# Performance work log

Hardware: AMD Instinct MI355X
Metric: run time of the kernel (lower is better)

Reference implementation:

```python
import jax, jax.numpy as jnp
import numpy as np


def setup_inputs() -> dict:
    key = jax.random.key(0)
    k1, k2 = jax.random.split(key)
    # x: [B, D, H, W, C] 3D latent grid, C == embedding_dim
    x = jax.random.normal(k1, (4, 32, 32, 16, 256), dtype=jnp.float32)
    # codebook stored as (embedding_dim, num_embeddings) like the TF variable
    embeddings = jax.random.uniform(k2, (256, 4096), dtype=jnp.float32)
    return {"x": x, "embeddings": embeddings}


def reference(x, embeddings):
    # Inference-mode forward of VectorQuantizer.call (training=False).
    D, K = embeddings.shape  # (embedding_dim, num_embeddings)
    flat = x.reshape(-1, D)  # [N, D]
    # squared L2 distances: ||z||^2 + ||e||^2 - 2 z.e  -> [N, K]
    sim = flat @ embeddings
    dist = (jnp.sum(flat * flat, axis=1, keepdims=True)
            + jnp.sum(embeddings * embeddings, axis=0)
            - 2.0 * sim)
    idx = jnp.argmin(dist, axis=1)  # [N]
    # nearest-codebook lookup (gather codebook columns)
    quantized = jnp.take(embeddings.T, idx, axis=0).reshape(x.shape)
    # perplexity from code usage histogram (avoids materializing [N,K] one-hot)
    n = flat.shape[0]
    counts = jnp.zeros((K,), dtype=jnp.float32).at[idx].add(1.0)
    avg_probs = counts / n
    perplexity = jnp.exp(-jnp.sum(avg_probs * jnp.log(avg_probs + 1e-10)))
    return quantized, perplexity
```

## Files before the change

### kernel.cpp

```cpp
#include <hip/hip_runtime.h>
#include <hip/hip_bf16.h>

#define NROWS 65536
#define DIM   256
#define KCB   4096
#define CHUNK 32
#define NCH   (KCB / CHUNK)
#define NBUF  4
#define BUFB  16384
#define NENHB 16384

typedef __attribute__((ext_vector_type(8))) short bf16x8;
typedef __attribute__((ext_vector_type(4))) float f32x4;

#define WAITV(n) asm volatile("s_waitcnt vmcnt(" #n ")" ::: "memory")

__device__ inline short f2bf(float f) {
    __hip_bfloat16 h = __float2bfloat16(f);
    return *reinterpret_cast<short*>(&h);
}

__global__ void prep_transpose(const float* __restrict__ E,
                               float* __restrict__ ET32,
                               ushort* __restrict__ ETbf)
{
    __shared__ float tile[64][65];
    const int kb = blockIdx.x * 64;
    const int db = blockIdx.y * 64;
    const int lo = threadIdx.x & 63;
    const int hi = threadIdx.x >> 6;

#pragma unroll
    for (int i = 0; i < 16; ++i) {
        int d = i * 4 + hi;
        tile[lo][d] = E[(size_t)(db + d) * KCB + kb + lo];
    }
    __syncthreads();
#pragma unroll
    for (int i = 0; i < 16; ++i) {
        int k = i * 4 + hi;
        float v = tile[k][lo];
        size_t off = (size_t)(kb + k) * DIM + db + lo;
        ET32[off] = v;
        ETbf[off] = (ushort)f2bf(v);
    }
}

__global__ void prep_enorm(const float* __restrict__ E, float* __restrict__ nenh)
{
    int k = blockIdx.x * 256 + threadIdx.x;
    float s = 0.0f;
#pragma unroll 8
    for (int d = 0; d < DIM; ++d) {
        float v = E[(size_t)d * KCB + k];
        s = fmaf(v, v, s);
    }
    nenh[k] = -0.5f * s;
}

__shared__ char lds_raw[NENHB + NBUF * BUFB];

template <int BUF>
__device__ __forceinline__ void stage_chunk(
    const char* __restrict__ etb, const int (&soff)[4], int wave, int ct)
{
    const char* base = etb + (size_t)ct * (CHUNK * 512);
#pragma unroll
    for (int j = 0; j < 4; ++j) {
        __builtin_amdgcn_global_load_lds(
            (const __attribute__((address_space(1))) unsigned*)(base + soff[j]),
            (__attribute__((address_space(3))) unsigned*)
                (lds_raw + NENHB + BUF * BUFB + wave * 4096 + j * 1024),
            16, 0, 0);
    }
}

template <int BUF>
__device__ __forceinline__ void process_chunk(
    const bf16x8 (&afrag)[2][8],
    const int (&boffB)[8],
    float (&best)[2][4], int (&bidx)[2][4],
    int l15, int ct)
{
    const float* nlds = (const float*)lds_raw;
#pragma unroll
    for (int tc = 0; tc < 2; ++tc) {
        const int col = ct * CHUNK + tc * 16 + l15;
        const float nh = nlds[ct * CHUNK + tc * 16 + l15];
        f32x4 acc0 = {nh, nh, nh, nh};
        f32x4 acc1 = {nh, nh, nh, nh};
        bf16x8 bfr[8];
#pragma unroll
        for (int kc = 0; kc < 8; ++kc)
            bfr[kc] = *(const bf16x8*)(lds_raw + boffB[kc]
                                       + BUF * BUFB + tc * 8192);
        __builtin_amdgcn_s_setprio(1);
#pragma unroll
        for (int kc = 0; kc < 8; ++kc) {
            acc0 = __builtin_amdgcn_mfma_f32_16x16x32_bf16(
                afrag[0][kc], bfr[kc], acc0, 0, 0, 0);
            acc1 = __builtin_amdgcn_mfma_f32_16x16x32_bf16(
                afrag[1][kc], bfr[kc], acc1, 0, 0, 0);
        }
        __builtin_amdgcn_s_setprio(0);
#pragma unroll
        for (int r = 0; r < 4; ++r) {
            float s0 = acc0[r];
            bool g0 = s0 > best[0][r];
            bidx[0][r] = g0 ? col : bidx[0][r];
            best[0][r] = fmaxf(best[0][r], s0);
            float s1 = acc1[r];
            bool g1 = s1 > best[1][r];
            bidx[1][r] = g1 ? col : bidx[1][r];
            best[1][r] = fmaxf(best[1][r], s1);
        }
    }
}

__global__ __launch_bounds__(256, 2)
void vq_argmin(const float* __restrict__ X,
               const ushort* __restrict__ ETbf,
               const float* __restrict__ nenh,
               int* __restrict__ idxout)
{
    const int tid  = threadIdx.x;
    const int lane = tid & 63;
    const int wave = tid >> 6;
    const int l15  = lane & 15;
    const int g    = lane >> 4;
    const int m    = l15 & 7;
    const long rowbase = (long)blockIdx.x * 128 + wave * 32;

    int soff[4];
#pragma unroll
    for (int j = 0; j < 4; ++j) {
        const int o    = wave * 4096 + j * 1024 + lane * 16;
        const int col0 = o >> 9;
        const int cph  = (o >> 4) & 31;
        soff[j] = (col0 << 9) + ((cph ^ (col0 & 7)) << 4);
    }

#pragma unroll
    for (int j = 0; j < 4; ++j) {
        int o = wave * 4096 + j * 1024 + lane * 16;
        __builtin_amdgcn_global_load_lds(
            (const __attribute__((address_space(1))) unsigned*)((const char*)nenh + o),
            (__attribute__((address_space(3))) unsigned*)
                (lds_raw + wave * 4096 + j * 1024),
            16, 0, 0);
    }
    stage_chunk<0>((const char*)ETbf, soff, wave, 0);
    stage_chunk<1>((const char*)ETbf, soff, wave, 1);
    stage_chunk<2>((const char*)ETbf, soff, wave, 2);

    bf16x8 afrag[2][8];
#pragma unroll
    for (int rt = 0; rt < 2; ++rt) {
        const float* xr = X + (rowbase + rt * 16 + l15) * DIM;
#pragma unroll
        for (int kc = 0; kc < 8; ++kc) {
            int k0 = g * 64 + kc * 8;
            float4 v0 = *(const float4*)(xr + k0);
            float4 v1 = *(const float4*)(xr + k0 + 4);
            bf16x8 f;
            f[0] = f2bf(v0.x); f[1] = f2bf(v0.y);
            f[2] = f2bf(v0.z); f[3] = f2bf(v0.w);
            f[4] = f2bf(v1.x); f[5] = f2bf(v1.y);
            f[6] = f2bf(v1.z); f[7] = f2bf(v1.w);
            afrag[rt][kc] = f;
        }
    }

    int boffB[8];
#pragma unroll
    for (int kc = 0; kc < 8; ++kc)
        boffB[kc] = NENHB + l15 * 512 + ((((g << 3) + kc) ^ m) << 4);

    float best[2][4];
    int   bidx[2][4];
#pragma unroll
    for (int rt = 0; rt < 2; ++rt)
#pragma unroll
        for (int r = 0; r < 4; ++r) { best[rt][r] = -3.4e38f; bidx[rt][r] = 0x7fffffff; }

    const char* etb = (const char*)ETbf;

    for (int gq = 0; gq < 31; ++gq) {
        const int ct = gq * 4;
        WAITV(8); __builtin_amdgcn_s_barrier();
        stage_chunk<3>(etb, soff, wave, ct + 3);
        process_chunk<0>(afrag, boffB, best, bidx, l15, ct);
        WAITV(8); __builtin_amdgcn_s_barrier();
        stage_chunk<0>(etb, soff, wave, ct + 4);
        process_chunk<1>(afrag, boffB, best, bidx, l15, ct + 1);
        WAITV(8); __builtin_amdgcn_s_barrier();
        stage_chunk<1>(etb, soff, wave, ct + 5);
        process_chunk<2>(afrag, boffB, best, bidx, l15, ct + 2);
        WAITV(8); __builtin_amdgcn_s_barrier();
        stage_chunk<2>(etb, soff, wave, ct + 6);
        process_chunk<3>(afrag, boffB, best, bidx, l15, ct + 3);
    }
    WAITV(8); __builtin_amdgcn_s_barrier();
    stage_chunk<3>(etb, soff, wave, 127);
    process_chunk<0>(afrag, boffB, best, bidx, l15, 124);
    WAITV(8); __builtin_amdgcn_s_barrier();
    process_chunk<1>(afrag, boffB, best, bidx, l15, 125);
    WAITV(4); __builtin_amdgcn_s_barrier();
    process_chunk<2>(afrag, boffB, best, bidx, l15, 126);
    WAITV(0); __builtin_amdgcn_s_barrier();
    process_chunk<3>(afrag, boffB, best, bidx, l15, 127);

#pragma unroll
    for (int rt = 0; rt < 2; ++rt) {
#pragma unroll
        for (int r = 0; r < 4; ++r) {
            float v = best[rt][r];
            int   ix = bidx[rt][r];
#pragma unroll
            for (int off = 1; off < 16; off <<= 1) {
                float ov = __shfl_xor(v, off, 64);
                int   oi = __shfl_xor(ix, off, 64);
                if (ov > v || (ov == v && oi < ix)) { v = ov; ix = oi; }
            }
            if (l15 == 0) {
                long row = rowbase + rt * 16 + g * 4 + r;
                idxout[row] = ix;
            }
        }
    }
}

__global__ void vq_gather(const int* __restrict__ idxin,
                          const float* __restrict__ ET32,
                          float* __restrict__ out,
                          unsigned* __restrict__ counts)
{
    const int tid = threadIdx.x;
    const long n  = (long)blockIdx.x * 4 + (tid >> 6);
    const int d4  = tid & 63;
    const int idx = idxin[n];
    float4 v = *(const float4*)(ET32 + (size_t)idx * DIM + d4 * 4);
    *(float4*)(out + n * DIM + d4 * 4) = v;
    if (d4 == 0) atomicAdd(&counts[idx], 1u);
}

__global__ void vq_perplexity(const unsigned* __restrict__ counts, float* __restrict__ outp)
{
    __shared__ float wsum[4];
    const int tid = threadIdx.x;
    float s = 0.0f;
    for (int k = tid; k < KCB; k += 256) {
        float p = (float)counts[k] * (1.0f / (float)NROWS);
        s += p * logf(p + 1e-10f);
    }
#pragma unroll
    for (int off = 32; off >= 1; off >>= 1) s += __shfl_down(s, off, 64);
    if ((tid & 63) == 0) wsum[tid >> 6] = s;
    __syncthreads();
    if (tid == 0) outp[0] = expf(-(wsum[0] + wsum[1] + wsum[2] + wsum[3]));
}

extern "C" void kernel_launch(void* const* d_in, const int* in_sizes, int n_in,
                              void* d_out, int out_size, void* d_ws, size_t ws_size,
                              hipStream_t stream)
{
    const float* X = (const float*)d_in[0];
    const float* E = (const float*)d_in[1];
    float* out = (float*)d_out;

    char* ws = (char*)d_ws;
    float*    ET32   = (float*)ws;
    ushort*   ETbf   = (ushort*)(ws + (size_t)KCB * DIM * 4);
    float*    nenh   = (float*)(ws + (size_t)KCB * DIM * 6);
    int*      idxbuf = (int*)(ws + (size_t)KCB * DIM * 6 + KCB * 4);
    unsigned* counts = (unsigned*)(ws + (size_t)KCB * DIM * 6 + KCB * 4 + NROWS * 4);

    hipMemsetAsync(counts, 0, KCB * sizeof(unsigned), stream);

    prep_transpose<<<dim3(KCB / 64, DIM / 64), dim3(256), 0, stream>>>(E, ET32, ETbf);
    prep_enorm<<<KCB / 256, dim3(256), 0, stream>>>(E, nenh);
    vq_argmin<<<NROWS / 128, dim3(256), 0, stream>>>(X, ETbf, nenh, idxbuf);
    vq_gather<<<NROWS / 4, dim3(256), 0, stream>>>(idxbuf, ET32, out, counts);
    vq_perplexity<<<1, dim3(256), 0, stream>>>(counts, out + (size_t)NROWS * DIM);
}
```

Before: 191.9 us.

## Software-pipeline LDS fragment reads with register double-buffering across chunk halves

```diff
diff --git a/kernel.cpp b/kernel.cpp
--- a/kernel.cpp
+++ b/kernel.cpp
@@ -8,12 +8,14 @@
 #define NCH   (KCB / CHUNK)
 #define NBUF  4
 #define BUFB  16384
-#define NENHB 16384
+#define NENH_BASE (NBUF * BUFB)
 
 typedef __attribute__((ext_vector_type(8))) short bf16x8;
 typedef __attribute__((ext_vector_type(4))) float f32x4;
 
-#define WAITV(n) asm volatile("s_waitcnt vmcnt(" #n ")" ::: "memory")
+#define WAITV0 asm volatile("s_waitcnt vmcnt(0)" ::: "memory")
+#define WAITV4 asm volatile("s_waitcnt vmcnt(4)" ::: "memory")
+#define WAITV8 asm volatile("s_waitcnt vmcnt(8)" ::: "memory")
 
 __device__ inline short f2bf(float f) {
     __hip_bfloat16 h = __float2bfloat16(f);
@@ -58,7 +60,7 @@
     nenh[k] = -0.5f * s;
 }
 
-__shared__ char lds_raw[NENHB + NBUF * BUFB];
+__shared__ char lds_raw[NBUF * BUFB + 16384];
 
 template <int BUF>
 __device__ __forceinline__ void stage_chunk(
@@ -70,51 +72,64 @@
         __builtin_amdgcn_global_load_lds(
             (const __attribute__((address_space(1))) unsigned*)(base + soff[j]),
             (__attribute__((address_space(3))) unsigned*)
-                (lds_raw + NENHB + BUF * BUFB + wave * 4096 + j * 1024),
+                (lds_raw + BUF * BUFB + wave * 4096 + j * 1024),
             16, 0, 0);
     }
 }
 
-template <int BUF>
-__device__ __forceinline__ void process_chunk(
+template <int BUF, int TC>
+__device__ __forceinline__ void read_batch(
+    const int (&boffB)[8], int nhbyte, bf16x8 (&bfr)[8], float& nh)
+{
+#pragma unroll
+    for (int kc = 0; kc < 8; ++kc)
+        bfr[kc] = *(const bf16x8*)(lds_raw + BUF * BUFB + TC * 8192 + boffB[kc]);
+    nh = *(const float*)(lds_raw + NENH_BASE + nhbyte);
+}
+
+__device__ __forceinline__ void mfma_cluster(
+    const bf16x8 (&afrag)[2][8], const bf16x8 (&bfr)[8], float nh,
+    float (&best)[2][4], int (&bidx)[2][4], int col)
+{
+    f32x4 acc0 = {nh, nh, nh, nh};
+    f32x4 acc1 = {nh, nh, nh, nh};
+    __builtin_amdgcn_s_setprio(1);
+#pragma unroll
+    for (int kc = 0; kc < 8; ++kc) {
+        acc0 = __builtin_amdgcn_mfma_f32_16x16x32_bf16(afrag[0][kc], bfr[kc], acc0, 0, 0, 0);
+        acc1 = __builtin_amdgcn_mfma_f32_16x16x32_bf16(afrag[1][kc], bfr[kc], acc1, 0, 0, 0);
+    }
+    __builtin_amdgcn_s_setprio(0);
+#pragma unroll
+    for (int r = 0; r < 4; ++r) {
+        float s0 = acc0[r];
+        bool g0 = s0 > best[0][r];
+        bidx[0][r] = g0 ? col : bidx[0][r];
+        best[0][r] = fmaxf(best[0][r], s0);
+        float s1 = acc1[r];
+        bool g1 = s1 > best[1][r];
+        bidx[1][r] = g1 ? col : bidx[1][r];
+        best[1][r] = fmaxf(best[1][r], s1);
+    }
+}
+
+template <int BUF, int WN, bool STG, bool RA>
+__device__ __forceinline__ void chunk_step(
+    const char* __restrict__ etb, const int (&soff)[4], int wave, int ct,
+    const int (&boffB)[8], int l15,
     const bf16x8 (&afrag)[2][8],
-    const int (&boffB)[8],
-    float (&best)[2][4], int (&bidx)[2][4],
-    int l15, int ct)
-{
-    const float* nlds = (const float*)lds_raw;
-#pragma unroll
-    for (int tc = 0; tc < 2; ++tc) {
-        const int col = ct * CHUNK + tc * 16 + l15;
-        const float nh = nlds[ct * CHUNK + tc * 16 + l15];
-        f32x4 acc0 = {nh, nh, nh, nh};
-        f32x4 acc1 = {nh, nh, nh, nh};
-        bf16x8 bfr[8];
-#pragma unroll
-        for (int kc = 0; kc < 8; ++kc)
-            bfr[kc] = *(const bf16x8*)(lds_raw + boffB[kc]
-                                       + BUF * BUFB + tc * 8192);
-        __builtin_amdgcn_s_setprio(1);
-#pragma unroll
-        for (int kc = 0; kc < 8; ++kc) {
-            acc0 = __builtin_amdgcn_mfma_f32_16x16x32_bf16(
-                afrag[0][kc], bfr[kc], acc0, 0, 0, 0);
-            acc1 = __builtin_amdgcn_mfma_f32_16x16x32_bf16(
-                afrag[1][kc], bfr[kc], acc1, 0, 0, 0);
-        }
-        __builtin_amdgcn_s_setprio(0);
-#pragma unroll
-        for (int r = 0; r < 4; ++r) {
-            float s0 = acc0[r];
-            bool g0 = s0 > best[0][r];
-            bidx[0][r] = g0 ? col : bidx[0][r];
-            best[0][r] = fmaxf(best[0][r], s0);
-            float s1 = acc1[r];
-            bool g1 = s1 > best[1][r];
-            bidx[1][r] = g1 ? col : bidx[1][r];
-            best[1][r] = fmaxf(best[1][r], s1);
-        }
-    }
+    bf16x8 (&bA)[8], bf16x8 (&bB)[8], float& nhA, float& nhB,
+    float (&best)[2][4], int (&bidx)[2][4])
+{
+    if constexpr (WN == 4) { WAITV4; } else { WAITV0; }
+    __builtin_amdgcn_s_barrier();
+    __builtin_amdgcn_sched_barrier(0);
+    if constexpr (STG) stage_chunk<(BUF + 3) & 3>(etb, soff, wave, ct + 3);
+    read_batch<BUF, 1>(boffB, ct * 128 + 64 + l15 * 4, bB, nhB);
+    mfma_cluster(afrag, bA, nhA, best, bidx, ct * CHUNK + l15);
+    if constexpr (RA)
+        read_batch<(BUF + 1) & 3, 0>(boffB, (ct + 1) * 128 + l15 * 4, bA, nhA);
+    mfma_cluster(afrag, bB, nhB, best, bidx, ct * CHUNK + 16 + l15);
 }
 
 __global__ __launch_bounds__(256, 2)
@@ -130,28 +145,7 @@
     const int g    = lane >> 4;
     const int m    = l15 & 7;
     const long rowbase = (long)blockIdx.x * 128 + wave * 32;
-
-    int soff[4];
-#pragma unroll
-    for (int j = 0; j < 4; ++j) {
-        const int o    = wave * 4096 + j * 1024 + lane * 16;
-        const int col0 = o >> 9;
-        const int cph  = (o >> 4) & 31;
-        soff[j] = (col0 << 9) + ((cph ^ (col0 & 7)) << 4);
-    }
-
-#pragma unroll
-    for (int j = 0; j < 4; ++j) {
-        int o = wave * 4096 + j * 1024 + lane * 16;
-        __builtin_amdgcn_global_load_lds(
-            (const __attribute__((address_space(1))) unsigned*)((const char*)nenh + o),
-            (__attribute__((address_space(3))) unsigned*)
-                (lds_raw + wave * 4096 + j * 1024),
-            16, 0, 0);
-    }
-    stage_chunk<0>((const char*)ETbf, soff, wave, 0);
-    stage_chunk<1>((const char*)ETbf, soff, wave, 1);
-    stage_chunk<2>((const char*)ETbf, soff, wave, 2);
+    const char* etb = (const char*)ETbf;
 
     bf16x8 afrag[2][8];
 #pragma unroll
@@ -171,10 +165,32 @@
         }
     }
 
+    int soff[4];
+#pragma unroll
+    for (int j = 0; j < 4; ++j) {
+        const int o    = wave * 4096 + j * 1024 + lane * 16;
+        const int col0 = o >> 9;
+        const int cph  = (o >> 4) & 31;
+        soff[j] = (col0 << 9) + ((cph ^ (col0 & 7)) << 4);
+    }
+
     int boffB[8];
 #pragma unroll
     for (int kc = 0; kc < 8; ++kc)
-        boffB[kc] = NENHB + l15 * 512 + ((((g << 3) + kc) ^ m) << 4);
+        boffB[kc] = l15 * 512 + ((((g << 3) + kc) ^ m) << 4);
+
+#pragma unroll
+    for (int j = 0; j < 4; ++j) {
+        int o = wave * 4096 + j * 1024 + lane * 16;
+        __builtin_amdgcn_global_load_lds(
+            (const __attribute__((address_space(1))) unsigned*)((const char*)nenh + o),
+            (__attribute__((address_space(3))) unsigned*)
+                (lds_raw + NENH_BASE + wave * 4096 + j * 1024),
+            16, 0, 0);
+    }
+    stage_chunk<0>(etb, soff, wave, 0);
+    stage_chunk<1>(etb, soff, wave, 1);
+    stage_chunk<2>(etb, soff, wave, 2);
 
     float best[2][4];
     int   bidx[2][4];
@@ -183,32 +199,33 @@
 #pragma unroll
         for (int r = 0; r < 4; ++r) { best[rt][r] = -3.4e38f; bidx[rt][r] = 0x7fffffff; }
 
-    const char* etb = (const char*)ETbf;
+    bf16x8 bA[8], bB[8];
+    float nhA, nhB;
+
+    WAITV8;
+    __builtin_amdgcn_s_barrier();
+    __builtin_amdgcn_sched_barrier(0);
+    read_batch<0, 0>(boffB, 0 + l15 * 4, bA, nhA);
 
     for (int gq = 0; gq < 31; ++gq) {
         const int ct = gq * 4;
-        WAITV(8); __builtin_amdgcn_s_barrier();
-        stage_chunk<3>(etb, soff, wave, ct + 3);
-        process_chunk<0>(afrag, boffB, best, bidx, l15, ct);
-        WAITV(8); __builtin_amdgcn_s_barrier();
-        stage_chunk<0>(etb, soff, wave, ct + 4);
-        process_chunk<1>(afrag, boffB, best, bidx, l15, ct + 1);
-        WAITV(8); __builtin_amdgcn_s_barrier();
-        stage_chunk<1>(etb, soff, wave, ct + 5);
-        process_chunk<2>(afrag, boffB, best, bidx, l15, ct + 2);
-        WAITV(8); __builtin_amdgcn_s_barrier();
-        stage_chunk<2>(etb, soff, wave, ct + 6);
-        process_chunk<3>(afrag, boffB, best, bidx, l15, ct + 3);
-    }
-    WAITV(8); __builtin_amdgcn_s_barrier();
-    stage_chunk<3>(etb, soff, wave, 127);
-    process_chunk<0>(afrag, boffB, best, bidx, l15, 124);
-    WAITV(8); __builtin_amdgcn_s_barrier();
-    process_chunk<1>(afrag, boffB, best, bidx, l15, 125);
-    WAITV(4); __builtin_amdgcn_s_barrier();
-    process_chunk<2>(afrag, boffB, best, bidx, l15, 126);
-    WAITV(0); __builtin_amdgcn_s_barrier();
-    process_chunk<3>(afrag, boffB, best, bidx, l15, 127);
+        chunk_step<0, 4, true, true>(etb, soff, wave, ct + 0, boffB, l15,
+                                     afrag, bA, bB, nhA, nhB, best, bidx);
+        chunk_step<1, 4, true, true>(etb, soff, wave, ct + 1, boffB, l15,
+                                     afrag, bA, bB, nhA, nhB, best, bidx);
+        chunk_step<2, 4, true, true>(etb, soff, wave, ct + 2, boffB, l15,
+                                     afrag, bA, bB, nhA, nhB, best, bidx);
+        chunk_step<3, 4, true, true>(etb, soff, wave, ct + 3, boffB, l15,
+                                     afrag, bA, bB, nhA, nhB, best, bidx);
+    }
+    chunk_step<0, 4, true,  true >(etb, soff, wave, 124, boffB, l15,
+                                   afrag, bA, bB, nhA, nhB, best, bidx);
+    chunk_step<1, 4, false, true >(etb, soff, wave, 125, boffB, l15,
+                                   afrag, bA, bB, nhA, nhB, best, bidx);
+    chunk_step<2, 0, false, true >(etb, soff, wave, 126, boffB, l15,
+                                   afrag, bA, bB, nhA, nhB, best, bidx);
+    chunk_step<3, 0, false, false>(etb, soff, wave, 127, boffB, l15,
+                                   afrag, bA, bB, nhA, nhB, best, bidx);
 
 #pragma unroll
     for (int rt = 0; rt < 2; ++rt) {
```

Result: faster. 182.2 us (-5.1%).
